# Performance work log

Hardware: AMD Instinct MI355X
Metric: run time of the kernel (lower is better)

The kernel has to match this reference:

```python
import jax, jax.numpy as jnp
import numpy as np

EPS = 1e-6
N_HEADS, N_KV = 16, 4


def rmsnorm(x, w):
    return x * jax.lax.rsqrt(jnp.mean(x * x, axis=-1, keepdims=True) + EPS) * w


def setup_inputs() -> dict:
    key = jax.random.key(0)
    ks = jax.random.split(key, 9)
    B, T, D, F = 2, 2048, 2048, 8192
    KVD = N_KV * (D // N_HEADS)
    s = lambda k, shape, fan: (jax.random.normal(k, shape, jnp.float32) * (fan ** -0.5))
    return {
        "x": jax.random.normal(ks[0], (B, T, D), jnp.float32),
        "norm1_w": jnp.ones((D,), jnp.float32),
        "norm2_w": jnp.ones((D,), jnp.float32),
        "Wq": s(ks[1], (D, D), D),
        "Wk": s(ks[2], (D, KVD), D),
        "Wv": s(ks[3], (D, KVD), D),
        "Wo": s(ks[4], (D, D), D),
        "Wc": s(ks[5], (D, D), D),
        "W1": s(ks[6], (D, F), D),
        "W2": s(ks[7], (F, D), F),
        "W3": s(ks[8], (D, F), D),
    }


def reference(x, norm1_w, norm2_w, Wq, Wk, Wv, Wo, Wc, W1, W2, W3):
    B, T, D = x.shape
    dh = D // N_HEADS          # 128
    G = N_HEADS // N_KV        # groups per kv head
    scale = dh ** -0.5

    xn = rmsnorm(x, norm1_w)
    q = xn @ Wq                               # [B,T,D]
    pos = q @ Wc                              # CoPE stand-in: contextual positional bias on Q
    q = (q + pos).reshape(B, T, N_KV, G, dh)  # group q heads under their kv head
    k = (xn @ Wk).reshape(B, T, N_KV, dh)
    v = (xn @ Wv).reshape(B, T, N_KV, dh)

    # GQA without repeat_interleave: contract each group against shared K/V
    scores = jnp.einsum('bqkgd,bskd->bkgqs', q, k) * scale   # [B,KV,G,T,T]
    i = jnp.arange(T)
    causal = i[:, None] >= i[None, :]
    scores = jnp.where(causal, scores, -jnp.inf)
    w = jax.nn.softmax(scores, axis=-1)
    att = jnp.einsum('bkgqs,bskd->bqkgd', w, v).reshape(B, T, D)

    x = x + att @ Wo
    xn2 = rmsnorm(x, norm2_w)
    x = x + (jax.nn.silu(xn2 @ W1) * (xn2 @ W3)) @ W2
    return x
```

## Files before the change

### kernel.cpp

```cpp
#include <hip/hip_runtime.h>
#include <hip/hip_bf16.h>

typedef __attribute__((ext_vector_type(8))) short short8;
typedef __attribute__((ext_vector_type(4))) float floatx4;
typedef unsigned short ushort_t;

__device__ inline float b2f(ushort_t s) {
    return __uint_as_float(((unsigned int)s) << 16);
}
__device__ inline ushort_t f2b(float f) {
    unsigned int u = __float_as_uint(f);
    unsigned int r = 0x7fff + ((u >> 16) & 1);
    return (ushort_t)((u + r) >> 16);
}
__device__ inline unsigned int cvtpk(float lo, float hi) {
    unsigned int r;
    asm("v_cvt_pk_bf16_f32 %0, %1, %2" : "=v"(r) : "v"(lo), "v"(hi));
    return r;
}
__device__ inline void load8(const float* p, float* f) {
    float4 a = *(const float4*)p;
    float4 b = *(const float4*)(p + 4);
    f[0] = a.x; f[1] = a.y; f[2] = a.z; f[3] = a.w;
    f[4] = b.x; f[5] = b.y; f[6] = b.z; f[7] = b.w;
}
__device__ inline void gload16(const ushort_t* g, ushort_t* l) {
    __builtin_amdgcn_global_load_lds(
        (const __attribute__((address_space(1))) unsigned int*)g,
        (__attribute__((address_space(3))) unsigned int*)l, 16, 0, 0);
}
__device__ inline void lbar() {
    asm volatile("s_waitcnt lgkmcnt(0)" ::: "memory");
    __builtin_amdgcn_s_barrier();
    asm volatile("" ::: "memory");
}

__global__ __launch_bounds__(256) void transpose_all(
    const float* __restrict__ s0, const float* __restrict__ s1,
    const float* __restrict__ s2, const float* __restrict__ s3,
    const float* __restrict__ s4, const float* __restrict__ s5,
    const float* __restrict__ s6, const float* __restrict__ s7,
    ushort_t* d0, ushort_t* d1, ushort_t* d2, ushort_t* d3,
    ushort_t* d4, ushort_t* d5, ushort_t* d6, ushort_t* d7) {
    int id = blockIdx.x;
    const float* src; ushort_t* dst; int K, N;
    if (id < 1024)       { src = s0; dst = d0; K = 2048; N = 2048; }
    else if (id < 1280)  { id -= 1024;  src = s1; dst = d1; K = 2048; N = 512; }
    else if (id < 1536)  { id -= 1280;  src = s2; dst = d2; K = 2048; N = 512; }
    else if (id < 2560)  { id -= 1536;  src = s3; dst = d3; K = 2048; N = 2048; }
    else if (id < 3584)  { id -= 2560;  src = s4; dst = d4; K = 2048; N = 2048; }
    else if (id < 7680)  { id -= 3584;  src = s5; dst = d5; K = 2048; N = 8192; }
    else if (id < 11776) { id -= 7680;  src = s6; dst = d6; K = 2048; N = 8192; }
    else                 { id -= 11776; src = s7; dst = d7; K = 8192; N = 2048; }
    int tn = N >> 6;
    int kb = (id / tn) * 64, nb = (id % tn) * 64;
    __shared__ ushort_t tile[64][65];
    int t = threadIdx.x;
#pragma unroll
    for (int i = 0; i < 4; ++i) {
        int r = (t >> 4) + i * 16;
        int c = (t & 15) * 4;
        float4 v = *(const float4*)(src + (size_t)(kb + r) * N + nb + c);
        tile[c + 0][r] = f2b(v.x);
        tile[c + 1][r] = f2b(v.y);
        tile[c + 2][r] = f2b(v.z);
        tile[c + 3][r] = f2b(v.w);
    }
    __syncthreads();
#pragma unroll
    for (int i = 0; i < 2; ++i) {
        int s = t + i * 256;
        int n = s >> 3, kc = (s & 7) * 8;
        ushort_t o[8];
#pragma unroll
        for (int j = 0; j < 8; ++j) o[j] = tile[n][kc + j];
        *(uint4*)(dst + (size_t)(nb + n) * K + kb + kc) = *(const uint4*)o;
    }
}

__global__ __launch_bounds__(256) void rmsnorm_kernel(const float* __restrict__ x,
                                                      const float* __restrict__ w,
                                                      ushort_t* __restrict__ out, int D) {
    int row = blockIdx.x;
    int t = threadIdx.x;
    const float* xr = x + (size_t)row * D;
    float f[8];
    load8(xr + t * 8, f);
    float ss = 0.f;
#pragma unroll
    for (int i = 0; i < 8; ++i) ss += f[i] * f[i];
#pragma unroll
    for (int m = 1; m < 64; m <<= 1) ss += __shfl_xor(ss, m);
    __shared__ float wsum[4];
    if ((t & 63) == 0) wsum[t >> 6] = ss;
    __syncthreads();
    float tot = wsum[0] + wsum[1] + wsum[2] + wsum[3];
    float r = rsqrtf(tot / (float)D + 1e-6f);
    float wf[8];
    load8(w + t * 8, wf);
    ushort_t o[8];
#pragma unroll
    for (int i = 0; i < 8; ++i) o[i] = f2b(f[i] * r * wf[i]);
    *(uint4*)(out + (size_t)row * D + t * 8) = *(const uint4*)o;
}

__global__ __launch_bounds__(256) void reduce_out(const ushort_t* __restrict__ p,
                                                  const float* __restrict__ resid,
                                                  float* __restrict__ out, int n) {
    int stride = gridDim.x * 256;
    for (int i = blockIdx.x * 256 + threadIdx.x; i * 8 < n; i += stride) {
        int i8 = i * 8;
        uint4 a = *(const uint4*)(p + i8);
        uint4 b = *(const uint4*)(p + n + i8);
        const ushort_t* ae = (const ushort_t*)&a;
        const ushort_t* be = (const ushort_t*)&b;
        float rr[8];
        load8(resid + i8, rr);
        float o[8];
#pragma unroll
        for (int j = 0; j < 8; ++j) o[j] = b2f(ae[j]) + b2f(be[j]) + rr[j];
        *(float4*)(out + i8) = make_float4(o[0], o[1], o[2], o[3]);
        *(float4*)(out + i8 + 4) = make_float4(o[4], o[5], o[6], o[7]);
    }
}

__device__ inline void vm6() { asm volatile("s_waitcnt vmcnt(6)" ::: "memory"); }
__device__ inline void vm4() { asm volatile("s_waitcnt vmcnt(4)" ::: "memory"); }

template <int MODE>
__global__ __launch_bounds__(512, 2) void gemm8(const ushort_t* __restrict__ A,
                                                const ushort_t* __restrict__ Bt,
                                                const ushort_t* __restrict__ aux,
                                                const float* __restrict__ aux2,
                                                void* __restrict__ Cv,
                                                void* __restrict__ C2v,
                                                void* __restrict__ C3v,
                                                int M, int N, int Ksub, int lda) {
    __shared__ __align__(16) ushort_t Lds[2 * 32768];
    const int tid = threadIdx.x;
    const int wv = tid >> 6, lane = tid & 63;
    const int l16 = lane & 15, l4 = lane >> 4;
    const int wr = wv >> 2, wc = wv & 3;
    int nwg = gridDim.x;
    int per = nwg >> 3;
    int wg = (blockIdx.x & 7) * per + (blockIdx.x >> 3);
    int mtiles = M >> 8;
    int bx = wg & (mtiles - 1);
    int by = wg / mtiles;
    int bm = bx << 8, bn = by << 8;
    int koff = blockIdx.y * Ksub;

    const int sr = tid >> 3;
    const int scol = (((tid & 7) ^ (sr & 7)) << 3);
    const ushort_t* gA = A + (size_t)(bm + sr) * lda + scol + koff;
    const ushort_t* gB = Bt + (size_t)(bn + sr) * lda + scol + koff;
    ushort_t* ldsw = Lds + wv * 512;

    const int ktiles = Ksub >> 6;
    const int niter = ktiles >> 1;
    const int km = ktiles - 1;

#define STG_A(slot, j, kt) gload16(gA + (size_t)((j) * 64) * lda + ((kt) << 6), ldsw + (slot) * 32768 + (j) * 4096)
#define STG_B(slot, j, kt) gload16(gB + (size_t)((j) * 64) * lda + ((kt) << 6), ldsw + (slot) * 32768 + 16384 + (j) * 4096)

    STG_A(0, 0, 0); STG_A(0, 2, 0); STG_A(0, 1, 0); STG_A(0, 3, 0);
    STG_B(0, 0, 0); STG_B(0, 1, 0); STG_B(0, 2, 0); STG_B(0, 3, 0);
    STG_A(1, 0, 1); STG_A(1, 2, 1);
    STG_B(1, 0, 1); STG_B(1, 1, 1); STG_B(1, 2, 1); STG_B(1, 3, 1);
    vm6();
    asm volatile("" ::: "memory");
    __builtin_amdgcn_s_barrier();

    const int lx = l4 ^ (l16 & 7);
    floatx4 acc[8][4] = {};
    short8 aR[4][2], bR[4][2];

#define DSA(slot, mh) { _Pragma("unroll") for (int m = 0; m < 4; ++m) { \
    _Pragma("unroll") for (int kk = 0; kk < 2; ++kk) \
      aR[m][kk] = *(const short8*)(Lds + (slot) * 32768 + \
          (wr * 128 + (mh) * 64 + m * 16 + l16) * 64 + ((lx ^ (kk << 2)) << 3)); } }
#define DSB(slot, nh) { _Pragma("unroll") for (int n = 0; n < 2; ++n) { \
    _Pragma("unroll") for (int kk = 0; kk < 2; ++kk) \
      bR[(nh) * 2 + n][kk] = *(const short8*)(Lds + (slot) * 32768 + 16384 + \
          (wc * 64 + ((nh) * 2 + n) * 16 + l16) * 64 + ((lx ^ (kk << 2)) << 3)); } }
#define QUAD(mh, nlo) { _Pragma("unroll") for (int m = 0; m < 4; ++m) \
    _Pragma("unroll") for (int n = 0; n < 2; ++n) \
    _Pragma("unroll") for (int kk = 0; kk < 2; ++kk) \
      acc[(mh) * 4 + m][(nlo) + n] = __builtin_amdgcn_mfma_f32_16x16x32_bf16( \
          aR[m][kk], bR[(nlo) + n][kk], acc[(mh) * 4 + m][(nlo) + n], 0, 0, 0); }
#define PHASE(DS, ST, MH, NLO, VM) { \
    DS; ST; \
    asm volatile("" ::: "memory"); \
    __builtin_amdgcn_s_barrier(); \
    asm volatile("s_waitcnt lgkmcnt(0)" ::: "memory"); \
    __builtin_amdgcn_sched_barrier(0); \
    __builtin_amdgcn_s_setprio(1); \
    QUAD(MH, NLO); \
    __builtin_amdgcn_s_setprio(0); \
    VM; \
    asm volatile("" ::: "memory"); \
    __builtin_amdgcn_s_barrier(); }

    for (int it = 0; it < niter; ++it) {
        int t1 = 2 * it + 1;
        int t2 = (2 * it + 2) & km;
        int t3 = (2 * it + 3) & km;
        PHASE({ DSA(0, 0); DSB(0, 0); }, { STG_A(1, 1, t1); STG_A(1, 3, t1); }, 0, 0, );
        PHASE({ DSB(0, 1); },            { STG_A(0, 0, t2); STG_A(0, 2, t2); }, 0, 2, );
        PHASE({ DSA(0, 1); },            { STG_B(0, 0, t2); STG_B(0, 1, t2); }, 1, 2, );
        PHASE({ },                       { STG_B(0, 2, t2); STG_B(0, 3, t2); }, 1, 0, vm6(); );
        PHASE({ DSA(1, 0); DSB(1, 0); }, { STG_A(0, 1, t2); STG_A(0, 3, t2); }, 0, 0, );
        PHASE({ DSB(1, 1); },            { STG_A(1, 0, t3); STG_A(1, 2, t3); }, 0, 2, );
        PHASE({ DSA(1, 1); },            { STG_B(1, 0, t3); STG_B(1, 1, t3); }, 1, 2, );
        PHASE({ },                       { STG_B(1, 2, t3); STG_B(1, 3, t3); }, 1, 0, vm6(); );
    }

#pragma unroll
    for (int mi = 0; mi < 8; ++mi)
#pragma unroll
        for (int ni = 0; ni < 4; ++ni)
#pragma unroll
            for (int r = 0; r < 4; ++r) {
                int row = bm + wr * 128 + mi * 16 + l4 * 4 + r;
                int col = bn + wc * 64 + ni * 16 + l16;
                size_t idx = (size_t)row * N + col;
                float v = acc[mi][ni][r];
                if (MODE == 0) {
                    ((ushort_t*)Cv)[idx] = f2b(v);
                } else if (MODE == 1) {
                    ((ushort_t*)Cv)[idx] = f2b(v + b2f(aux[idx]));
                } else if (MODE == 2) {
                    float h = b2f(aux[idx]);
                    ((ushort_t*)Cv)[idx] = f2b((h / (1.f + __expf(-h))) * v);
                } else if (MODE == 3) {
                    ((ushort_t*)Cv)[(size_t)blockIdx.y * M * N + idx] = f2b(v);
                } else if (MODE == 5) {
                    ((float*)Cv)[idx] = v + aux2[idx];
                } else if (MODE == 6) {
                    if (bn < 2048) {
                        ((ushort_t*)Cv)[(size_t)row * 2048 + col] = f2b(v);
                    } else if (bn < 2560) {
                        ((ushort_t*)C2v)[(size_t)row * 512 + (col - 2048)] = f2b(v);
                    } else {
                        ((ushort_t*)C3v)[(size_t)(col - 2560) * 4096 + row] = f2b(v);
                    }
                }
            }
#undef STG_A
#undef STG_B
#undef DSA
#undef DSB
#undef QUAD
#undef PHASE
}

template <int MODE>
__global__ __launch_bounds__(512, 1) void gemm8h(const ushort_t* __restrict__ A,
                                                 const ushort_t* __restrict__ Bt,
                                                 const ushort_t* __restrict__ aux,
                                                 const float* __restrict__ aux2,
                                                 void* __restrict__ Cv,
                                                 int M, int N, int K) {
    __shared__ __align__(16) ushort_t Lds[2 * 24576];
    const int tid = threadIdx.x;
    const int wv = tid >> 6, lane = tid & 63;
    const int l16 = lane & 15, l4 = lane >> 4;
    const int wr = wv >> 2, wc = wv & 3;
    int nwg = gridDim.x;
    int per = nwg >> 3;
    int wg = (blockIdx.x & 7) * per + (blockIdx.x >> 3);
    int mtiles = M >> 7;
    int bx = wg & (mtiles - 1);
    int by = wg / mtiles;
    int bm = bx << 7, bn = by << 8;

    const int sr = tid >> 3;
    const int scol = (((tid & 7) ^ (sr & 7)) << 3);
    const ushort_t* gA = A + (size_t)(bm + sr) * K + scol;
    const ushort_t* gB = Bt + (size_t)(bn + sr) * K + scol;
    ushort_t* ldsw = Lds + wv * 512;

    const int ktiles = K >> 6;
    const int niter = ktiles >> 1;
    const int km = ktiles - 1;

#define HSTG_A(slot, j, kt) gload16(gA + (size_t)((j) * 64) * K + ((kt) << 6), ldsw + (slot) * 24576 + (j) * 4096)
#define HSTG_B(slot, j, kt) gload16(gB + (size_t)((j) * 64) * K + ((kt) << 6), ldsw + (slot) * 24576 + 8192 + (j) * 4096)

    HSTG_A(0, 0, 0); HSTG_A(0, 1, 0);
    HSTG_B(0, 0, 0); HSTG_B(0, 1, 0); HSTG_B(0, 2, 0); HSTG_B(0, 3, 0);
    HSTG_A(1, 0, 1); HSTG_A(1, 1, 1);
    HSTG_B(1, 0, 1); HSTG_B(1, 1, 1);
    vm4();
    asm volatile("" ::: "memory");
    __builtin_amdgcn_s_barrier();

    const int lx = l4 ^ (l16 & 7);
    floatx4 acc[4][4] = {};
    short8 aR[2][2], bR[4][2];

#define HDSA(slot, mh) { _Pragma("unroll") for (int m = 0; m < 2; ++m) { \
    _Pragma("unroll") for (int kk = 0; kk < 2; ++kk) \
      aR[m][kk] = *(const short8*)(Lds + (slot) * 24576 + \
          (wr * 64 + (mh) * 32 + m * 16 + l16) * 64 + ((lx ^ (kk << 2)) << 3)); } }
#define HDSB(slot, nh) { _Pragma("unroll") for (int n = 0; n < 2; ++n) { \
    _Pragma("unroll") for (int kk = 0; kk < 2; ++kk) \
      bR[(nh) * 2 + n][kk] = *(const short8*)(Lds + (slot) * 24576 + 8192 + \
          (wc * 64 + ((nh) * 2 + n) * 16 + l16) * 64 + ((lx ^ (kk << 2)) << 3)); } }
#define HQUAD(mh, nlo) { _Pragma("unroll") for (int m = 0; m < 2; ++m) \
    _Pragma("unroll") for (int n = 0; n < 2; ++n) \
    _Pragma("unroll") for (int kk = 0; kk < 2; ++kk) \
      acc[(mh) * 2 + m][(nlo) + n] = __builtin_amdgcn_mfma_f32_16x16x32_bf16( \
          aR[m][kk], bR[(nlo) + n][kk], acc[(mh) * 2 + m][(nlo) + n], 0, 0, 0); }
#define HPHASE(DS, ST, MH, NLO, VM) { \
    DS; ST; \
    asm volatile("" ::: "memory"); \
    __builtin_amdgcn_s_barrier(); \
    asm volatile("s_waitcnt lgkmcnt(0)" ::: "memory"); \
    __builtin_amdgcn_sched_barrier(0); \
    __builtin_amdgcn_s_setprio(1); \
    HQUAD(MH, NLO); \
    __builtin_amdgcn_s_setprio(0); \
    VM; \
    asm volatile("" ::: "memory"); \
    __builtin_amdgcn_s_barrier(); }

    for (int it = 0; it < niter; ++it) {
        int t1 = 2 * it + 1;
        int t2 = (2 * it + 2) & km;
        int t3 = (2 * it + 3) & km;
        HPHASE({ HDSA(0, 0); HDSB(0, 0); }, { HSTG_B(1, 2, t1); HSTG_B(1, 3, t1); }, 0, 0, );
        HPHASE({ HDSB(0, 1); },             { },                                     0, 2, );
        HPHASE({ HDSA(0, 1); },             { HSTG_B(0, 0, t2); HSTG_B(0, 1, t2); }, 1, 2, );
        HPHASE({ },                         { HSTG_B(0, 2, t2); HSTG_B(0, 3, t2); }, 1, 0, vm4(); );
        HPHASE({ HDSA(1, 0); HDSB(1, 0); }, { HSTG_A(0, 0, t2); HSTG_A(0, 1, t2); }, 0, 0, );
        HPHASE({ HDSB(1, 1); },             { },                                     0, 2, );
        HPHASE({ HDSA(1, 1); },             { HSTG_B(1, 0, t3); HSTG_B(1, 1, t3); }, 1, 2, );
        HPHASE({ },                         { HSTG_A(1, 0, t3); HSTG_A(1, 1, t3); }, 1, 0, vm4(); );
    }

#pragma unroll
    for (int mi = 0; mi < 4; ++mi)
#pragma unroll
        for (int ni = 0; ni < 4; ++ni)
#pragma unroll
            for (int r = 0; r < 4; ++r) {
                int row = bm + wr * 64 + mi * 16 + l4 * 4 + r;
                int col = bn + wc * 64 + ni * 16 + l16;
                size_t idx = (size_t)row * N + col;
                float v = acc[mi][ni][r];
                if (MODE == 1) ((ushort_t*)Cv)[idx] = f2b(v + b2f(aux[idx]));
                else if (MODE == 5) ((float*)Cv)[idx] = v + aux2[idx];
            }
#undef HSTG_A
#undef HSTG_B
#undef HDSA
#undef HDSB
#undef HQUAD
#undef HPHASE
}

#define QB 256
#define SB 64

__global__ __launch_bounds__(512, 1) void attn_kernel(const ushort_t* __restrict__ Q,
                                                      const ushort_t* __restrict__ Kb,
                                                      const ushort_t* __restrict__ VbT,
                                                      ushort_t* __restrict__ O, int Tlen) {
    const int D = 2048, KVD = 512, dh = 128;
    const int MTOK = 4096;
    int p = blockIdx.x, h = blockIdx.y, b = blockIdx.z;
    int kv = h >> 2;
    int t = threadIdx.x, wave = t >> 6, lane = t & 63;
    int l16 = lane & 15, l4 = lane >> 4;
    __shared__ __align__(16) ushort_t LdsAll[45056];
    const float scale = 0.08838834764831845f;
    const ushort_t* Kg = Kb + ((size_t)(b * Tlen) + (t >> 4)) * KVD + kv * dh + (t & 15) * 8;
    const ushort_t* Vg = VbT + (size_t)(kv * dh + (t >> 3)) * MTOK + b * Tlen + (t & 7) * 8;
    const int kw_off = (t >> 4) * 136 + (t & 15) * 8;
    const int vw_off = 17408 + (t >> 3) * 72 + (t & 7) * 8;
    unsigned int* PsB = (unsigned int*)(LdsAll + 26624);

    for (int side = 0; side < 2; ++side) {
        int qt = side ? p : (7 - p);
        int qbase = qt * QB;
        int qw = qbase + wave * 32;
        short8 qf[2][4];
#pragma unroll
        for (int f = 0; f < 2; ++f) {
            const ushort_t* Qrow = Q + ((size_t)(b * Tlen) + qw + f * 16 + l16) * D + h * dh;
#pragma unroll
            for (int kk = 0; kk < 4; ++kk) qf[f][kk] = *(const short8*)(Qrow + kk * 32 + l4 * 8);
        }
        floatx4 o_acc[2][8] = {};
        float m_s[2], l_s[2];
#pragma unroll
        for (int f = 0; f < 2; ++f) { m_s[f] = -INFINITY; l_s[f] = 0.f; }
        int nst = 4 * qt + 4;
        uint4 kreg[2], vreg[2];
#pragma unroll
        for (int p4 = 0; p4 < 2; ++p4) {
            kreg[p4] = *(const uint4*)(Kg + (size_t)(p4 * 32) * KVD);
            vreg[p4] = *(const uint4*)(Vg + (size_t)(p4 * 64) * MTOK);
        }
        lbar();
#pragma unroll
        for (int p4 = 0; p4 < 2; ++p4)
            *(uint4*)(LdsAll + kw_off + p4 * 32 * 136) = kreg[p4];
        if (nst > 1) {
#pragma unroll
            for (int p4 = 0; p4 < 2; ++p4)
                kreg[p4] = *(const uint4*)(Kg + (size_t)(SB + p4 * 32) * KVD);
        }
        for (int st = 0; st < nst; ++st) {
            int cur = st & 1;
            int s0 = st * SB;
            lbar();
#pragma unroll
            for (int p4 = 0; p4 < 2; ++p4)
                *(uint4*)(LdsAll + vw_off + p4 * 64 * 72) = vreg[p4];
            if (st + 1 < nst) {
#pragma unroll
                for (int p4 = 0; p4 < 2; ++p4)
                    *(uint4*)(LdsAll + (cur ^ 1) * 8704 + kw_off + p4 * 32 * 136) = kreg[p4];
            }
            if (st + 1 < nst) {
                size_t off = (size_t)(st + 1) * SB;
#pragma unroll
                for (int p4 = 0; p4 < 2; ++p4)
                    vreg[p4] = *(const uint4*)(Vg + (size_t)(p4 * 64) * MTOK + off);
            }
            if (st + 2 < nst) {
                size_t off = (size_t)(st + 2) * SB;
#pragma unroll
                for (int p4 = 0; p4 < 2; ++p4)
                    kreg[p4] = *(const uint4*)(Kg + (off + p4 * 32) * KVD);
            }
            floatx4 sa[2][4] = {};
            __builtin_amdgcn_s_setprio(1);
#pragma unroll
            for (int ss = 0; ss < 4; ++ss)
#pragma unroll
                for (int kk = 0; kk < 4; ++kk) {
                    short8 kf = *(const short8*)(LdsAll + cur * 8704 + (ss * 16 + l16) * 136 + kk * 32 + l4 * 8);
                    sa[0][ss] = __builtin_amdgcn_mfma_f32_16x16x32_bf16(kf, qf[0][kk], sa[0][ss], 0, 0, 0);
                    sa[1][ss] = __builtin_amdgcn_mfma_f32_16x16x32_bf16(kf, qf[1][kk], sa[1][ss], 0, 0, 0);
                }
            __builtin_amdgcn_s_setprio(0);
            short8 pa[2][2];
#pragma unroll
            for (int f = 0; f < 2; ++f) {
                int qcol = qw + f * 16 + l16;
                float sv[4][4];
                float pmax = -INFINITY;
#pragma unroll
                for (int ss = 0; ss < 4; ++ss)
#pragma unroll
                    for (int r = 0; r < 4; ++r) {
                        int krow = s0 + ss * 16 + l4 * 4 + r;
                        float v = sa[f][ss][r] * scale;
                        if (krow > qcol) v = -INFINITY;
                        sv[ss][r] = v;
                        pmax = fmaxf(pmax, v);
                    }
                pmax = fmaxf(pmax, __shfl_xor(pmax, 16));
                pmax = fmaxf(pmax, __shfl_xor(pmax, 32));
                bool skip = __all(pmax <= m_s[f] + 8.f);
                float mn = skip ? m_s[f] : fmaxf(m_s[f], pmax);
                float rsum = 0.f;
#pragma unroll
                for (int ss = 0; ss < 4; ++ss)
#pragma unroll
                    for (int r = 0; r < 4; ++r) {
                        float pv = __expf(sv[ss][r] - mn);
                        sv[ss][r] = pv;
                        rsum += pv;
                    }
                rsum += __shfl_xor(rsum, 16);
                rsum += __shfl_xor(rsum, 32);
                if (skip) {
                    l_s[f] += rsum;
                } else {
                    float esc = __expf(m_s[f] - mn);
                    l_s[f] = l_s[f] * esc + rsum;
                    m_s[f] = mn;
                    float ef[4];
#pragma unroll
                    for (int r = 0; r < 4; ++r) ef[r] = __shfl(esc, l4 * 4 + r);
#pragma unroll
                    for (int c = 0; c < 8; ++c)
#pragma unroll
                        for (int r = 0; r < 4; ++r) o_acc[f][c][r] *= ef[r];
                }
                unsigned int* Pw = PsB + (wave * 2 + f) * 16 * 36;
#pragma unroll
                for (int ss = 0; ss < 4; ++ss) {
                    uint2 pk;
                    pk.x = cvtpk(sv[ss][0], sv[ss][1]);
                    pk.y = cvtpk(sv[ss][2], sv[ss][3]);
                    *(uint2*)&Pw[l16 * 36 + ss * 8 + l4 * 2] = pk;
                }
#pragma unroll
                for (int kk = 0; kk < 2; ++kk) {
                    uint4 pv4 = *(const uint4*)&Pw[l16 * 36 + kk * 16 + l4 * 4];
                    pa[f][kk] = *(const short8*)&pv4;
                }
            }
            lbar();
            __builtin_amdgcn_s_setprio(1);
#pragma unroll
            for (int c = 0; c < 8; ++c)
#pragma unroll
                for (int kk = 0; kk < 2; ++kk) {
                    short8 vf = *(const short8*)(LdsAll + 17408 + (c * 16 + l16) * 72 + kk * 32 + l4 * 8);
                    o_acc[0][c] = __builtin_amdgcn_mfma_f32_16x16x32_bf16(pa[0][kk], vf, o_acc[0][c], 0, 0, 0);
                    o_acc[1][c] = __builtin_amdgcn_mfma_f32_16x16x32_bf16(pa[1][kk], vf, o_acc[1][c], 0, 0, 0);
                }
            __builtin_amdgcn_s_setprio(0);
        }
        lbar();
        ushort_t* Osh = LdsAll;
#pragma unroll
        for (int f = 0; f < 2; ++f) {
            float linv[4];
#pragma unroll
            for (int r = 0; r < 4; ++r) linv[r] = 1.f / __shfl(l_s[f], l4 * 4 + r);
#pragma unroll
            for (int c = 0; c < 8; ++c)
#pragma unroll
                for (int r = 0; r < 4; ++r)
                    Osh[(wave * 32 + f * 16 + l4 * 4 + r) * 136 + c * 16 + l16] =
                        f2b(o_acc[f][c][r] * linv[r]);
        }
        lbar();
        {
            int orow = t >> 1, occ = (t & 1) * 64;
            const ushort_t* srcp = Osh + orow * 136 + occ;
            ushort_t* dstp = O + ((size_t)(b * Tlen) + qbase + orow) * D + h * dh + occ;
#pragma unroll
            for (int k = 0; k < 8; ++k)
                *(uint4*)(dstp + k * 8) = *(const uint4*)(srcp + k * 8);
        }
    }
}

extern "C" void kernel_launch(void* const* d_in, const int* in_sizes, int n_in,
                              void* d_out, int out_size, void* d_ws, size_t ws_size,
                              hipStream_t stream) {
    const float* x   = (const float*)d_in[0];
    const float* n1w = (const float*)d_in[1];
    const float* n2w = (const float*)d_in[2];
    const float* Wq  = (const float*)d_in[3];
    const float* Wk  = (const float*)d_in[4];
    const float* Wv  = (const float*)d_in[5];
    const float* Wo  = (const float*)d_in[6];
    const float* Wc  = (const float*)d_in[7];
    const float* W1  = (const float*)d_in[8];
    const float* W2  = (const float*)d_in[9];
    const float* W3  = (const float*)d_in[10];
    float* out = (float*)d_out;

    const int B = 2, T = 2048, D = 2048, F = 8192, KVD = 512;
    const int M = B * T;
    const size_t XD   = (size_t)M * D * 2;
    const size_t XDF  = (size_t)M * D * 4;
    const size_t KVSZ = (size_t)M * KVD * 2;
    const size_t MF   = (size_t)M * F * 2;
    const size_t WDD  = (size_t)D * D * 2;
    const size_t WQKV = (size_t)(D + 2 * KVD) * D * 2;
    const size_t WDF  = (size_t)D * F * 2;

    char* w = (char*)d_ws;
    ushort_t* xn    = (ushort_t*)(w);
    ushort_t* qtmp  = (ushort_t*)(w + XD);
    ushort_t* qfin  = (ushort_t*)(w + 2 * XD);
    float*    x2f   = (float*)   (w + 3 * XD);
    ushort_t* kbuf  = (ushort_t*)(w + 3 * XD + XDF);
    ushort_t* vbufT = (ushort_t*)(w + 3 * XD + XDF + KVSZ);
    ushort_t* h1    = (ushort_t*)(w + 3 * XD + XDF + 2 * KVSZ);
    char* wt = w + 3 * XD + XDF + 2 * KVSZ + MF;
    ushort_t* WqkvT = (ushort_t*)(wt);
    ushort_t* WcT   = (ushort_t*)(wt + WQKV);
    ushort_t* WoT   = (ushort_t*)(wt + WQKV + WDD);
    ushort_t* W1T   = (ushort_t*)(wt + WQKV + 2 * WDD);
    ushort_t* W3T   = (ushort_t*)(wt + WQKV + 2 * WDD + WDF);
    ushort_t* W2T   = (ushort_t*)(wt + WQKV + 2 * WDD + 2 * WDF);

    dim3 blk(256);
    dim3 blk8(512);

    transpose_all<<<15872, blk, 0, stream>>>(
        Wq, Wk, Wv, Wc, Wo, W1, W3, W2,
        WqkvT, WqkvT + (size_t)2048 * D, WqkvT + (size_t)2560 * D,
        WcT, WoT, W1T, W3T, W2T);

    rmsnorm_kernel<<<M, blk, 0, stream>>>(x, n1w, xn, D);
    gemm8<6><<<dim3((M / 256) * (3072 / 256)), blk8, 0, stream>>>(
        xn, WqkvT, nullptr, nullptr, qtmp, kbuf, vbufT, M, 3072, D, D);
    gemm8h<1><<<dim3((M / 128) * (D / 256)), blk8, 0, stream>>>(
        qtmp, WcT, qtmp, nullptr, qfin, M, D, D);
    attn_kernel<<<dim3(8, 16, B), blk8, 0, stream>>>(qfin, kbuf, vbufT, qtmp, T);
    gemm8h<5><<<dim3((M / 128) * (D / 256)), blk8, 0, stream>>>(
        qtmp, WoT, nullptr, x, x2f, M, D, D);
    rmsnorm_kernel<<<M, blk, 0, stream>>>(x2f, n2w, xn, D);
    gemm8<0><<<dim3((M / 256) * (F / 256)), blk8, 0, stream>>>(
        xn, W1T, nullptr, nullptr, h1, nullptr, nullptr, M, F, D, D);
    gemm8<2><<<dim3((M / 256) * (F / 256)), blk8, 0, stream>>>(
        xn, W3T, h1, nullptr, h1, nullptr, nullptr, M, F, D, D);
    gemm8<3><<<dim3((M / 256) * (D / 256), 2), blk8, 0, stream>>>(
        h1, W2T, nullptr, nullptr, xn, nullptr, nullptr, M, D, F / 2, F);
    reduce_out<<<1024, blk, 0, stream>>>(xn, x2f, out, M * D);
}
```

Measured before the change: 785.9 us.

## Split attention KV range across paired blocks and merge partial softmax results

```diff
diff --git a/kernel.cpp b/kernel.cpp
--- a/kernel.cpp
+++ b/kernel.cpp
@@ -122,6 +122,33 @@
         *(float4*)(out + i8) = make_float4(o[0], o[1], o[2], o[3]);
         *(float4*)(out + i8 + 4) = make_float4(o[4], o[5], o[6], o[7]);
     }
+}
+
+__global__ __launch_bounds__(256) void attn_merge(const ushort_t* __restrict__ Pb,
+                                                  const float* __restrict__ Mb,
+                                                  const float* __restrict__ Lb,
+                                                  ushort_t* __restrict__ out) {
+    const int PSZ = 32 * 2048 * 128;
+    int t = threadIdx.x;
+    int r = blockIdx.x * 16 + (t >> 4);
+    int d0 = (t & 15) * 8;
+    float m1 = Mb[r], l1 = Lb[r];
+    float m2 = Mb[65536 + r], l2 = Lb[65536 + r];
+    float ms = fmaxf(m1, m2);
+    float w1 = l1 * __expf(m1 - ms);
+    float w2 = l2 * __expf(m2 - ms);
+    float inv = 1.f / (w1 + w2);
+    w1 *= inv; w2 *= inv;
+    uint4 a = *(const uint4*)(Pb + (size_t)r * 128 + d0);
+    uint4 b = *(const uint4*)(Pb + (size_t)PSZ + (size_t)r * 128 + d0);
+    const ushort_t* ae = (const ushort_t*)&a;
+    const ushort_t* be = (const ushort_t*)&b;
+    int bh = r >> 11, qrow = r & 2047;
+    int bb = bh >> 4, h = bh & 15;
+    ushort_t o[8];
+#pragma unroll
+    for (int j = 0; j < 8; ++j) o[j] = f2b(b2f(ae[j]) * w1 + b2f(be[j]) * w2);
+    *(uint4*)(out + ((size_t)(bb * 2048 + qrow) * 2048) + h * 128 + d0) = *(const uint4*)o;
 }
 
 __device__ inline void vm6() { asm volatile("s_waitcnt vmcnt(6)" ::: "memory"); }
@@ -366,10 +393,14 @@
 __global__ __launch_bounds__(512, 1) void attn_kernel(const ushort_t* __restrict__ Q,
                                                       const ushort_t* __restrict__ Kb,
                                                       const ushort_t* __restrict__ VbT,
-                                                      ushort_t* __restrict__ O, int Tlen) {
+                                                      ushort_t* __restrict__ Pb,
+                                                      float* __restrict__ Mb,
+                                                      float* __restrict__ Lb, int Tlen) {
     const int D = 2048, KVD = 512, dh = 128;
     const int MTOK = 4096;
+    const int PSZ = 32 * 2048 * 128;
     int p = blockIdx.x, h = blockIdx.y, b = blockIdx.z;
+    int jsp = (p >= 4) ? 1 : 0;
     int kv = h >> 2;
     int t = threadIdx.x, wave = t >> 6, lane = t & 63;
     int l16 = lane & 15, l4 = lane >> 4;
@@ -383,6 +414,7 @@
 
     for (int side = 0; side < 2; ++side) {
         int qt = side ? p : (7 - p);
+        if (qt >= 8) qt -= 8;
         int qbase = qt * QB;
         int qw = qbase + wave * 32;
         short8 qf[2][4];
@@ -395,42 +427,45 @@
         floatx4 o_acc[2][8] = {};
         float m_s[2], l_s[2];
 #pragma unroll
-        for (int f = 0; f < 2; ++f) { m_s[f] = -INFINITY; l_s[f] = 0.f; }
-        int nst = 4 * qt + 4;
+        for (int f = 0; f < 2; ++f) { m_s[f] = -1e30f; l_s[f] = 0.f; }
+        int half = 2 * qt + 2;
+        int st0 = jsp * half;
+        int stEnd = st0 + half;
         uint4 kreg[2], vreg[2];
 #pragma unroll
         for (int p4 = 0; p4 < 2; ++p4) {
-            kreg[p4] = *(const uint4*)(Kg + (size_t)(p4 * 32) * KVD);
-            vreg[p4] = *(const uint4*)(Vg + (size_t)(p4 * 64) * MTOK);
+            kreg[p4] = *(const uint4*)(Kg + (size_t)((size_t)st0 * SB + p4 * 32) * KVD);
+            vreg[p4] = *(const uint4*)(Vg + (size_t)(p4 * 64) * MTOK + (size_t)st0 * SB);
         }
         lbar();
 #pragma unroll
         for (int p4 = 0; p4 < 2; ++p4)
-            *(uint4*)(LdsAll + kw_off + p4 * 32 * 136) = kreg[p4];
-        if (nst > 1) {
+            *(uint4*)(LdsAll + (st0 & 1) * 8704 + kw_off + p4 * 32 * 136) = kreg[p4];
+        {
+            size_t off = (size_t)(st0 + 1) * SB;
 #pragma unroll
             for (int p4 = 0; p4 < 2; ++p4)
-                kreg[p4] = *(const uint4*)(Kg + (size_t)(SB + p4 * 32) * KVD);
+                kreg[p4] = *(const uint4*)(Kg + (off + p4 * 32) * KVD);
         }
-        for (int st = 0; st < nst; ++st) {
+        for (int st = st0; st < stEnd; ++st) {
             int cur = st & 1;
             int s0 = st * SB;
             lbar();
 #pragma unroll
             for (int p4 = 0; p4 < 2; ++p4)
                 *(uint4*)(LdsAll + vw_off + p4 * 64 * 72) = vreg[p4];
-            if (st + 1 < nst) {
+            if (st + 1 < stEnd) {
 #pragma unroll
                 for (int p4 = 0; p4 < 2; ++p4)
                     *(uint4*)(LdsAll + (cur ^ 1) * 8704 + kw_off + p4 * 32 * 136) = kreg[p4];
             }
-            if (st + 1 < nst) {
+            if (st + 1 < stEnd) {
                 size_t off = (size_t)(st + 1) * SB;
 #pragma unroll
                 for (int p4 = 0; p4 < 2; ++p4)
                     vreg[p4] = *(const uint4*)(Vg + (size_t)(p4 * 64) * MTOK + off);
             }
-            if (st + 2 < nst) {
+            if (st + 2 < stEnd) {
                 size_t off = (size_t)(st + 2) * SB;
 #pragma unroll
                 for (int p4 = 0; p4 < 2; ++p4)
@@ -519,12 +554,23 @@
             __builtin_amdgcn_s_setprio(0);
         }
         lbar();
+#pragma unroll
+        for (int f = 0; f < 2; ++f) {
+            if (l4 == 0) {
+                int ridx = jsp * 65536 + ((b * 16 + h) << 11) + qw + f * 16 + l16;
+                Mb[ridx] = m_s[f];
+                Lb[ridx] = l_s[f];
+            }
+        }
         ushort_t* Osh = LdsAll;
 #pragma unroll
         for (int f = 0; f < 2; ++f) {
             float linv[4];
 #pragma unroll
-            for (int r = 0; r < 4; ++r) linv[r] = 1.f / __shfl(l_s[f], l4 * 4 + r);
+            for (int r = 0; r < 4; ++r) {
+                float lv = __shfl(l_s[f], l4 * 4 + r);
+                linv[r] = (lv > 0.f) ? (1.f / lv) : 0.f;
+            }
 #pragma unroll
             for (int c = 0; c < 8; ++c)
 #pragma unroll
@@ -536,7 +582,8 @@
         {
             int orow = t >> 1, occ = (t & 1) * 64;
             const ushort_t* srcp = Osh + orow * 136 + occ;
-            ushort_t* dstp = O + ((size_t)(b * Tlen) + qbase + orow) * D + h * dh + occ;
+            ushort_t* dstp = Pb + (size_t)jsp * PSZ +
+                             ((size_t)((b * 16 + h)) * 2048 + qbase + orow) * 128 + occ;
 #pragma unroll
             for (int k = 0; k < 8; ++k)
                 *(uint4*)(dstp + k * 8) = *(const uint4*)(srcp + k * 8);
@@ -585,6 +632,9 @@
     ushort_t* W1T   = (ushort_t*)(wt + WQKV + 2 * WDD);
     ushort_t* W3T   = (ushort_t*)(wt + WQKV + 2 * WDD + WDF);
     ushort_t* W2T   = (ushort_t*)(wt + WQKV + 2 * WDD + 2 * WDF);
+    ushort_t* Pb = h1;
+    float*    Mb = (float*)((char*)h1 + 2 * (size_t)32 * 2048 * 128 * 2);
+    float*    Lb = Mb + 2 * 65536;
 
     dim3 blk(256);
     dim3 blk8(512);
@@ -599,7 +649,8 @@
         xn, WqkvT, nullptr, nullptr, qtmp, kbuf, vbufT, M, 3072, D, D);
     gemm8h<1><<<dim3((M / 128) * (D / 256)), blk8, 0, stream>>>(
         qtmp, WcT, qtmp, nullptr, qfin, M, D, D);
-    attn_kernel<<<dim3(8, 16, B), blk8, 0, stream>>>(qfin, kbuf, vbufT, qtmp, T);
+    attn_kernel<<<dim3(8, 16, B), blk8, 0, stream>>>(qfin, kbuf, vbufT, Pb, Mb, Lb, T);
+    attn_merge<<<4096, blk, 0, stream>>>(Pb, Mb, Lb, qtmp);
     gemm8h<5><<<dim3((M / 128) * (D / 256)), blk8, 0, stream>>>(
         qtmp, WoT, nullptr, x, x2f, M, D, D);
     rmsnorm_kernel<<<M, blk, 0, stream>>>(x2f, n2w, xn, D);
```

Result: faster. 736.2 us (-6.3%).
